# Kernel tuning notes

Measured on AMD Instinct MI355X. Metric: run time of the kernel, lower is better.

Reference implementation:

```python
import jax, jax.numpy as jnp
import numpy as np

NUM_EMBEDDINGS = 2048
EMBEDDING_DIM = 512
INPUT_DIM = 256  # input_chan**2 = 16**2
COMMITMENT_COST = 0.25
BN_EPS = 1e-5


def setup_inputs() -> dict:
    key = jax.random.key(0)
    ks = jax.random.split(key, 8)
    B, N = 64, 1024
    inputs = jax.random.normal(ks[0], (B, N, INPUT_DIM), dtype=jnp.float32)
    # embedding init: uniform(-1/K, 1/K) as in the torch module
    emb_scale = 1.0 / NUM_EMBEDDINGS
    embedding = jax.random.uniform(ks[1], (NUM_EMBEDDINGS, EMBEDDING_DIM), dtype=jnp.float32,
                                   minval=-emb_scale, maxval=emb_scale)
    # Linear layers use torch convention W[out, in]
    W1 = jax.random.normal(ks[2], (EMBEDDING_DIM, INPUT_DIM), dtype=jnp.float32) / np.sqrt(INPUT_DIM)
    b1 = jnp.zeros((EMBEDDING_DIM,), dtype=jnp.float32)
    W2 = jax.random.normal(ks[3], (INPUT_DIM, EMBEDDING_DIM), dtype=jnp.float32) / np.sqrt(EMBEDDING_DIM)
    b2 = jnp.zeros((INPUT_DIM,), dtype=jnp.float32)
    # BatchNorm affine params initialized to 1/0 as in the module
    bn1_gamma = jnp.ones((INPUT_DIM,), dtype=jnp.float32)
    bn1_beta = jnp.zeros((INPUT_DIM,), dtype=jnp.float32)
    bn2_gamma = jnp.ones((EMBEDDING_DIM,), dtype=jnp.float32)
    bn2_beta = jnp.zeros((EMBEDDING_DIM,), dtype=jnp.float32)
    return {"inputs": inputs, "bn1_gamma": bn1_gamma, "bn1_beta": bn1_beta,
            "W1": W1, "b1": b1, "embedding": embedding,
            "bn2_gamma": bn2_gamma, "bn2_beta": bn2_beta, "W2": W2, "b2": b2}


def reference(inputs, bn1_gamma, bn1_beta, W1, b1, embedding, bn2_gamma, bn2_beta, W2, b2):
    sg = jax.lax.stop_gradient
    input_shape = inputs.shape
    flat = inputs.reshape(-1, INPUT_DIM)  # [T, D_in]
    # BatchNorm1d in eval mode (running_mean=0, running_var=1); Dropout is identity in eval.
    bn1_scale = 1.0 / jnp.sqrt(1.0 + BN_EPS)
    x = flat * (bn1_gamma * bn1_scale) + bn1_beta
    x = x @ W1.T + b1  # [T, E]
    # pairwise squared distances to codebook, argmin
    distances = (jnp.sum(x * x, axis=1, keepdims=True)
                 + jnp.sum(embedding * embedding, axis=1)
                 - 2.0 * x @ embedding.T)  # [T, K]
    encoding_indices = jnp.argmin(distances, axis=1)  # [T]
    # gather == one-hot @ embedding (same math, same gradient scatter-add)
    quantized = jnp.take(embedding, encoding_indices, axis=0)  # [T, E]
    bn2_scale = 1.0 / jnp.sqrt(1.0 + BN_EPS)
    quantized = quantized * (bn2_gamma * bn2_scale) + bn2_beta
    quantized = (quantized @ W2.T + b2).reshape(input_shape)
    e_latent_loss = jnp.mean((sg(quantized) - inputs) ** 2)
    q_latent_loss = jnp.mean((quantized - sg(inputs)) ** 2)
    loss = q_latent_loss + COMMITMENT_COST * e_latent_loss
    quantized_st = inputs + sg(quantized - inputs)  # straight-through
    T = flat.shape[0]
    usage = jnp.zeros((NUM_EMBEDDINGS,), dtype=jnp.float32).at[encoding_indices].add(1.0) / T
    return (loss, quantized_st, usage)
```

## Files before the change

### kernel.cpp

```cpp
#include <hip/hip_runtime.h>
#include <math.h>
#include <stdint.h>

#define TOK 65536
#define DIN 256
#define EDIM 512
#define KCB 2048
#define NTB 128

#define OFF_MP   0u
#define OFF_CP   524288u
#define OFF_Q    526336u
#define OFF_W2T  1050624u
#define OFF_U    1181696u
#define OFF_CQ   1182208u
#define OFF_BH   1182464u
#define TOT_F    1444608u

typedef short short8 __attribute__((ext_vector_type(8)));
typedef float f32x4 __attribute__((ext_vector_type(4)));

__device__ __forceinline__ unsigned short bf16rne(float x) {
    uint32_t u = __float_as_uint(x);
    u += 0x7fffu + ((u >> 16) & 1u);
    return (unsigned short)(u >> 16);
}

__global__ void prep1_kernel(const float* __restrict__ W1, const float* __restrict__ W2,
                             const float* __restrict__ bn1_beta, const float* __restrict__ bn2_gamma,
                             const float* __restrict__ bn2_beta, const float* __restrict__ b2,
                             float* __restrict__ W2T, float* __restrict__ u, float* __restrict__ cQ,
                             float* __restrict__ out) {
    __shared__ float red[256];
    const int b = blockIdx.x, t = threadIdx.x;
    const int gid = b * 256 + t;
    if (gid == 0) out[0] = 0.0f;
    if (gid < KCB) out[1 + TOK * DIN + gid] = 0.0f;
    const float s = 1.0f / sqrtf(1.0f + 1e-5f);
    if (b < EDIM) {
        int e = b;
        W2T[e * DIN + t] = bn2_gamma[e] * s * W2[t * EDIM + e];
        float v = bn1_beta[t] * W1[e * DIN + t];
        red[t] = v; __syncthreads();
        for (int off = 128; off; off >>= 1) { if (t < off) red[t] += red[t + off]; __syncthreads(); }
        if (t == 0) u[e] = red[0];
    } else {
        int o = b - EDIM;
        float v = bn2_beta[t] * W2[o * EDIM + t] + bn2_beta[t + 256] * W2[o * EDIM + t + 256];
        red[t] = v; __syncthreads();
        for (int off = 128; off; off >>= 1) { if (t < off) red[t] += red[t + off]; __syncthreads(); }
        if (t == 0) cQ[o] = b2[o] + red[0];
    }
}

__global__ __launch_bounds__(512) void prep2_kernel(const float* __restrict__ E, const float* __restrict__ W1,
                                                    const float* __restrict__ W2T, const float* __restrict__ bn1_gamma,
                                                    const float* __restrict__ cQ, const float* __restrict__ b1,
                                                    const float* __restrict__ u,
                                                    float* __restrict__ Q, float* __restrict__ cp,
                                                    unsigned short* __restrict__ Bh) {
    __shared__ __align__(16) unsigned short hs[8][264];
    const int t = threadIdx.x;
    const int col = t & 255;
    const int half = __builtin_amdgcn_readfirstlane(t >> 8);
    const int k0 = blockIdx.x * 8;
    const float* __restrict__ Ek = E + ((size_t)k0 + (size_t)half * 4) * EDIM;

    float m[4] = {0, 0, 0, 0};
    float q[4] = {0, 0, 0, 0};
    for (int e0 = 0; e0 < EDIM; e0 += 8) {
        float w1v[8], w2v[8];
#pragma unroll
        for (int j = 0; j < 8; j++) {
            w1v[j] = W1[(e0 + j) * DIN + col];
            w2v[j] = W2T[(e0 + j) * DIN + col];
        }
#pragma unroll
        for (int r = 0; r < 4; r++) {
#pragma unroll
            for (int j = 0; j < 8; j++) {
                float ev = Ek[(size_t)r * EDIM + e0 + j];
                m[r] += ev * w1v[j];
                q[r] += ev * w2v[j];
            }
        }
    }
    const float s = 1.0f / sqrtf(1.0f + 1e-5f);
    const float gs = bn1_gamma[col] * s;
    const float cq = cQ[col];
#pragma unroll
    for (int r = 0; r < 4; r++) {
        Q[(size_t)(k0 + half * 4 + r) * DIN + col] = q[r] + cq;
        hs[half * 4 + r][col] = bf16rne(gs * m[r]);
    }

    {
        const int wv = t >> 6, l = t & 63;
        const float* __restrict__ Er = E + (size_t)(k0 + wv) * EDIM;
        float sa = 0.0f, sb = 0.0f;
#pragma unroll
        for (int i = 0; i < 8; i++) {
            int e = l + i * 64;
            float ev = Er[e];
            float be = b1[e] + u[e];
            sa += ev * be; sb += ev * ev;
        }
        float v = sa - 0.5f * sb;
#pragma unroll
        for (int off = 32; off; off >>= 1) v += __shfl_down(v, off, 64);
        if (l == 0) cp[k0 + wv] = v;
    }

    __syncthreads();

    if (t < 256) {
        const int rr = t & 7, qr = (t >> 3) & 3, kc = t >> 5;
        const int nt = k0 >> 4;
        const int l2 = (k0 & 8) + rr + (qr << 4);
        short8 vh = *(const short8*)&hs[rr][kc * 32 + qr * 8];
        *(short8*)&Bh[((size_t)kc * NTB + nt) * 512 + (size_t)l2 * 8] = vh;
    }
}

__global__ __launch_bounds__(256, 2) void score_fused_kernel(const float* __restrict__ flat,
                                                             const unsigned short* __restrict__ Bh,
                                                             const float* __restrict__ cp,
                                                             const float* __restrict__ Q,
                                                             float* __restrict__ out) {
    __shared__ float mv[2][128];
    __shared__ int   mi[2][128];
    const int t = threadIdx.x, lane = t & 63, w = t >> 6;
    const int wr = w >> 1, wc = w & 1;
    const int m0 = blockIdx.x * 128;
    const int fr = lane & 15, qr = lane >> 4;

    short8 af[8][4];
#pragma unroll
    for (int kc = 0; kc < 8; kc++)
#pragma unroll
        for (int mt = 0; mt < 4; mt++) {
            int row = m0 + wr * 64 + mt * 16 + fr;
            const float* p = flat + (size_t)row * DIN + kc * 32 + qr * 8;
            float4 a = *(const float4*)p;
            float4 b = *(const float4*)(p + 4);
            float f[8] = {a.x, a.y, a.z, a.w, b.x, b.y, b.z, b.w};
            unsigned short* hp = (unsigned short*)&af[kc][mt];
#pragma unroll
            for (int j = 0; j < 8; j++) hp[j] = bf16rne(f[j]);
        }

    const unsigned short* __restrict__ Bhaving = Bh + ((size_t)(wc * 64)) * 512 + (size_t)lane * 8;

    float bestv[4][4];
    int besti[4][4];
#pragma unroll
    for (int mt = 0; mt < 4; mt++)
#pragma unroll
        for (int r = 0; r < 4; r++) { bestv[mt][r] = -3.4e38f; besti[mt][r] = 0; }

    const f32x4 ZERO4 = {0.f, 0.f, 0.f, 0.f};

    short8 bf[8];
#pragma unroll
    for (int kc = 0; kc < 8; kc++)
        bf[kc] = *(const short8*)(Bhaving + ((size_t)kc * NTB) * 512);

#pragma unroll 1
    for (int nt = 0; nt < 64; nt++) {
        f32x4 acc[4];
        acc[0] = __builtin_amdgcn_mfma_f32_16x16x32_bf16(af[0][0], bf[0], ZERO4, 0, 0, 0);
        acc[1] = __builtin_amdgcn_mfma_f32_16x16x32_bf16(af[0][1], bf[0], ZERO4, 0, 0, 0);
        acc[2] = __builtin_amdgcn_mfma_f32_16x16x32_bf16(af[0][2], bf[0], ZERO4, 0, 0, 0);
        acc[3] = __builtin_amdgcn_mfma_f32_16x16x32_bf16(af[0][3], bf[0], ZERO4, 0, 0, 0);
#pragma unroll
        for (int kc = 1; kc < 4; kc++) {
#pragma unroll
            for (int mt = 0; mt < 4; mt++)
                acc[mt] = __builtin_amdgcn_mfma_f32_16x16x32_bf16(af[kc][mt], bf[kc], acc[mt], 0, 0, 0);
        }
        if (nt < 63) {
#pragma unroll
            for (int kc = 0; kc < 4; kc++)
                bf[kc] = *(const short8*)(Bhaving + ((size_t)kc * NTB + nt + 1) * 512);
        }
#pragma unroll
        for (int kc = 4; kc < 8; kc++) {
#pragma unroll
            for (int mt = 0; mt < 4; mt++)
                acc[mt] = __builtin_amdgcn_mfma_f32_16x16x32_bf16(af[kc][mt], bf[kc], acc[mt], 0, 0, 0);
        }
        if (nt < 63) {
#pragma unroll
            for (int kc = 4; kc < 8; kc++)
                bf[kc] = *(const short8*)(Bhaving + ((size_t)kc * NTB + nt + 1) * 512);
        }
        const int base = wc * 1024 + nt * 16 + fr;
        const float cpv = cp[base];
#pragma unroll
        for (int mt = 0; mt < 4; mt++)
#pragma unroll
            for (int r = 0; r < 4; r++) {
                float v = acc[mt][r] + cpv;
                if (v > bestv[mt][r]) { bestv[mt][r] = v; besti[mt][r] = base; }
            }
    }

#pragma unroll
    for (int mt = 0; mt < 4; mt++)
#pragma unroll
        for (int r = 0; r < 4; r++) {
            float bv = bestv[mt][r];
            int bc = besti[mt][r];
#pragma unroll
            for (int xm = 1; xm < 16; xm <<= 1) {
                float ov = __shfl_xor(bv, xm, 64);
                int oc = __shfl_xor(bc, xm, 64);
                if (ov > bv || (ov == bv && oc < bc)) { bv = ov; bc = oc; }
            }
            if (fr == 0) {
                int rl = wr * 64 + mt * 16 + qr * 4 + r;
                mv[wc][rl] = bv;
                mi[wc][rl] = bc;
            }
        }
    __syncthreads();

    float lsum = 0.0f;
    for (int rr = 0; rr < 32; rr++) {
        int rl = w * 32 + rr;
        int row = m0 + rl;
        float v0 = mv[0][rl], v1 = mv[1][rl];
        int c0 = mi[0][rl], c1 = mi[1][rl];
        int k = (v1 > v0 || (v1 == v0 && c1 < c0)) ? c1 : c0;
        const float* qr_ = Q + (size_t)k * DIN;
        const float* xr = flat + (size_t)row * DIN;
        float* ob = out + 1 + (size_t)row * DIN;
#pragma unroll
        for (int cc = 0; cc < 4; cc++) {
            int j = lane + 64 * cc;
            float q = qr_[j];
            float d = q - xr[j];
            lsum += d * d;
            ob[j] = q;
        }
        if (lane == 0) atomicAdd(out + 1 + TOK * DIN + k, 1.0f / (float)TOK);
    }
#pragma unroll
    for (int off = 32; off; off >>= 1) lsum += __shfl_down(lsum, off, 64);
    if (lane == 0) atomicAdd(out, lsum * (1.25f / (float)((size_t)TOK * DIN)));
}

extern "C" void kernel_launch(void* const* d_in, const int* in_sizes, int n_in,
                              void* d_out, int out_size, void* d_ws, size_t ws_size,
                              hipStream_t stream) {
    const float* inputs = (const float*)d_in[0];
    const float* bn1_gamma = (const float*)d_in[1];
    const float* bn1_beta  = (const float*)d_in[2];
    const float* W1 = (const float*)d_in[3];
    const float* b1 = (const float*)d_in[4];
    const float* E  = (const float*)d_in[5];
    const float* bn2_gamma = (const float*)d_in[6];
    const float* bn2_beta  = (const float*)d_in[7];
    const float* W2 = (const float*)d_in[8];
    const float* b2 = (const float*)d_in[9];

    float* ws = (float*)d_ws;
    float* cp  = ws + OFF_CP;
    float* Q   = ws + OFF_Q;
    float* W2T = ws + OFF_W2T;
    float* u   = ws + OFF_U;
    float* cQ  = ws + OFF_CQ;
    unsigned short* Bh = (unsigned short*)(ws + OFF_BH);
    float* out = (float*)d_out;

    hipLaunchKernelGGL(prep1_kernel, dim3(768), dim3(256), 0, stream,
                       W1, W2, bn1_beta, bn2_gamma, bn2_beta, b2, W2T, u, cQ, out);
    hipLaunchKernelGGL(prep2_kernel, dim3(256), dim3(512), 0, stream,
                       E, W1, W2T, bn1_gamma, cQ, b1, u, Q, cp, Bh);
    hipLaunchKernelGGL(score_fused_kernel, dim3(512), dim3(256), 0, stream,
                       inputs, Bh, cp, Q, out);
}
```

Before: 272.7 us.

## Shrink score tile to 16 rows per wave across full codebook, raise occupancy

Each wave now computes scores for 16 token rows against all 2048 codes instead of 64 rows against half the codebook. This removes the cross-wave LDS argmin merge and its barrier, cuts the register footprint, and allows 4 blocks per CU with twice the grid. In exchange each B fragment load feeds only one MFMA instead of four, so codebook traffic from L2 rises substantially. A single dependent accumulator chain also reduces MFMA-level parallelism per wave.

```diff
diff --git a/kernel.cpp b/kernel.cpp
--- a/kernel.cpp
+++ b/kernel.cpp
@@ -122,128 +122,105 @@
     }
 }
 
-__global__ __launch_bounds__(256, 2) void score_fused_kernel(const float* __restrict__ flat,
+__global__ __launch_bounds__(256, 4) void score_fused_kernel(const float* __restrict__ flat,
                                                              const unsigned short* __restrict__ Bh,
                                                              const float* __restrict__ cp,
                                                              const float* __restrict__ Q,
                                                              float* __restrict__ out) {
-    __shared__ float mv[2][128];
-    __shared__ int   mi[2][128];
     const int t = threadIdx.x, lane = t & 63, w = t >> 6;
-    const int wr = w >> 1, wc = w & 1;
-    const int m0 = blockIdx.x * 128;
+    const int m0 = blockIdx.x * 64;
     const int fr = lane & 15, qr = lane >> 4;
 
-    short8 af[8][4];
+    short8 af[8];
+#pragma unroll
+    for (int kc = 0; kc < 8; kc++) {
+        int row = m0 + w * 16 + fr;
+        const float* p = flat + (size_t)row * DIN + kc * 32 + qr * 8;
+        float4 a = *(const float4*)p;
+        float4 b = *(const float4*)(p + 4);
+        float f[8] = {a.x, a.y, a.z, a.w, b.x, b.y, b.z, b.w};
+        unsigned short* hp = (unsigned short*)&af[kc];
+#pragma unroll
+        for (int j = 0; j < 8; j++) hp[j] = bf16rne(f[j]);
+    }
+
+    const unsigned short* __restrict__ Bbase = Bh + (size_t)lane * 8;
+
+    float bestv[4];
+    int besti[4];
+#pragma unroll
+    for (int r = 0; r < 4; r++) { bestv[r] = -3.4e38f; besti[r] = 0; }
+
+    const f32x4 ZERO4 = {0.f, 0.f, 0.f, 0.f};
+
+    short8 bf[8];
 #pragma unroll
     for (int kc = 0; kc < 8; kc++)
-#pragma unroll
-        for (int mt = 0; mt < 4; mt++) {
-            int row = m0 + wr * 64 + mt * 16 + fr;
-            const float* p = flat + (size_t)row * DIN + kc * 32 + qr * 8;
-            float4 a = *(const float4*)p;
-            float4 b = *(const float4*)(p + 4);
-            float f[8] = {a.x, a.y, a.z, a.w, b.x, b.y, b.z, b.w};
-            unsigned short* hp = (unsigned short*)&af[kc][mt];
-#pragma unroll
-            for (int j = 0; j < 8; j++) hp[j] = bf16rne(f[j]);
-        }
-
-    const unsigned short* __restrict__ Bhaving = Bh + ((size_t)(wc * 64)) * 512 + (size_t)lane * 8;
-
-    float bestv[4][4];
-    int besti[4][4];
-#pragma unroll
-    for (int mt = 0; mt < 4; mt++)
-#pragma unroll
-        for (int r = 0; r < 4; r++) { bestv[mt][r] = -3.4e38f; besti[mt][r] = 0; }
-
-    const f32x4 ZERO4 = {0.f, 0.f, 0.f, 0.f};
-
-    short8 bf[8];
-#pragma unroll
-    for (int kc = 0; kc < 8; kc++)
-        bf[kc] = *(const short8*)(Bhaving + ((size_t)kc * NTB) * 512);
+        bf[kc] = *(const short8*)(Bbase + ((size_t)kc * NTB) * 512);
 
 #pragma unroll 1
-    for (int nt = 0; nt < 64; nt++) {
-        f32x4 acc[4];
-        acc[0] = __builtin_amdgcn_mfma_f32_16x16x32_bf16(af[0][0], bf[0], ZERO4, 0, 0, 0);
-        acc[1] = __builtin_amdgcn_mfma_f32_16x16x32_bf16(af[0][1], bf[0], ZERO4, 0, 0, 0);
-        acc[2] = __builtin_amdgcn_mfma_f32_16x16x32_bf16(af[0][2], bf[0], ZERO4, 0, 0, 0);
-        acc[3] = __builtin_amdgcn_mfma_f32_16x16x32_bf16(af[0][3], bf[0], ZERO4, 0, 0, 0);
-#pragma unroll
-        for (int kc = 1; kc < 4; kc++) {
-#pragma unroll
-            for (int mt = 0; mt < 4; mt++)
-                acc[mt] = __builtin_amdgcn_mfma_f32_16x16x32_bf16(af[kc][mt], bf[kc], acc[mt], 0, 0, 0);
-        }
-        if (nt < 63) {
+    for (int nt = 0; nt < 128; nt++) {
+        f32x4 acc;
+        acc = __builtin_amdgcn_mfma_f32_16x16x32_bf16(af[0], bf[0], ZERO4, 0, 0, 0);
+#pragma unroll
+        for (int kc = 1; kc < 4; kc++)
+            acc = __builtin_amdgcn_mfma_f32_16x16x32_bf16(af[kc], bf[kc], acc, 0, 0, 0);
+        if (nt < 127) {
 #pragma unroll
             for (int kc = 0; kc < 4; kc++)
-                bf[kc] = *(const short8*)(Bhaving + ((size_t)kc * NTB + nt + 1) * 512);
-        }
-#pragma unroll
-        for (int kc = 4; kc < 8; kc++) {
-#pragma unroll
-            for (int mt = 0; mt < 4; mt++)
-                acc[mt] = __builtin_amdgcn_mfma_f32_16x16x32_bf16(af[kc][mt], bf[kc], acc[mt], 0, 0, 0);
-        }
-        if (nt < 63) {
+                bf[kc] = *(const short8*)(Bbase + ((size_t)kc * NTB + nt + 1) * 512);
+        }
+#pragma unroll
+        for (int kc = 4; kc < 8; kc++)
+            acc = __builtin_amdgcn_mfma_f32_16x16x32_bf16(af[kc], bf[kc], acc, 0, 0, 0);
+        if (nt < 127) {
 #pragma unroll
             for (int kc = 4; kc < 8; kc++)
-                bf[kc] = *(const short8*)(Bhaving + ((size_t)kc * NTB + nt + 1) * 512);
-        }
-        const int base = wc * 1024 + nt * 16 + fr;
+                bf[kc] = *(const short8*)(Bbase + ((size_t)kc * NTB + nt + 1) * 512);
+        }
+        const int base = nt * 16 + fr;
         const float cpv = cp[base];
 #pragma unroll
-        for (int mt = 0; mt < 4; mt++)
-#pragma unroll
-            for (int r = 0; r < 4; r++) {
-                float v = acc[mt][r] + cpv;
-                if (v > bestv[mt][r]) { bestv[mt][r] = v; besti[mt][r] = base; }
+        for (int r = 0; r < 4; r++) {
+            float v = acc[r] + cpv;
+            if (v > bestv[r]) { bestv[r] = v; besti[r] = base; }
+        }
+    }
+
+#pragma unroll
+    for (int r = 0; r < 4; r++) {
+        float bv = bestv[r];
+        int bc = besti[r];
+#pragma unroll
+        for (int xm = 1; xm < 16; xm <<= 1) {
+            float ov = __shfl_xor(bv, xm, 64);
+            int oc = __shfl_xor(bc, xm, 64);
+            if (ov > bv || (ov == bv && oc < bc)) { bv = ov; bc = oc; }
+        }
+        besti[r] = bc;
+    }
+
+    float lsum = 0.0f;
+#pragma unroll
+    for (int rq = 0; rq < 4; rq++) {
+#pragma unroll
+        for (int r = 0; r < 4; r++) {
+            int rr = rq * 4 + r;
+            int row = m0 + w * 16 + rr;
+            int k = __shfl(besti[r], rq * 16, 64);
+            const float* qr_ = Q + (size_t)k * DIN;
+            const float* xr = flat + (size_t)row * DIN;
+            float* ob = out + 1 + (size_t)row * DIN;
+#pragma unroll
+            for (int cc = 0; cc < 4; cc++) {
+                int j = lane + 64 * cc;
+                float q = qr_[j];
+                float d = q - xr[j];
+                lsum += d * d;
+                ob[j] = q;
             }
-    }
-
-#pragma unroll
-    for (int mt = 0; mt < 4; mt++)
-#pragma unroll
-        for (int r = 0; r < 4; r++) {
-            float bv = bestv[mt][r];
-            int bc = besti[mt][r];
-#pragma unroll
-            for (int xm = 1; xm < 16; xm <<= 1) {
-                float ov = __shfl_xor(bv, xm, 64);
-                int oc = __shfl_xor(bc, xm, 64);
-                if (ov > bv || (ov == bv && oc < bc)) { bv = ov; bc = oc; }
-            }
-            if (fr == 0) {
-                int rl = wr * 64 + mt * 16 + qr * 4 + r;
-                mv[wc][rl] = bv;
-                mi[wc][rl] = bc;
-            }
-        }
-    __syncthreads();
-
-    float lsum = 0.0f;
-    for (int rr = 0; rr < 32; rr++) {
-        int rl = w * 32 + rr;
-        int row = m0 + rl;
-        float v0 = mv[0][rl], v1 = mv[1][rl];
-        int c0 = mi[0][rl], c1 = mi[1][rl];
-        int k = (v1 > v0 || (v1 == v0 && c1 < c0)) ? c1 : c0;
-        const float* qr_ = Q + (size_t)k * DIN;
-        const float* xr = flat + (size_t)row * DIN;
-        float* ob = out + 1 + (size_t)row * DIN;
-#pragma unroll
-        for (int cc = 0; cc < 4; cc++) {
-            int j = lane + 64 * cc;
-            float q = qr_[j];
-            float d = q - xr[j];
-            lsum += d * d;
-            ob[j] = q;
-        }
-        if (lane == 0) atomicAdd(out + 1 + TOK * DIN + k, 1.0f / (float)TOK);
+            if (lane == 0) atomicAdd(out + 1 + TOK * DIN + k, 1.0f / (float)TOK);
+        }
     }
 #pragma unroll
     for (int off = 32; off; off >>= 1) lsum += __shfl_down(lsum, off, 64);
@@ -277,6 +254,6 @@
                        W1, W2, bn1_beta, bn2_gamma, bn2_beta, b2, W2T, u, cQ, out);
     hipLaunchKernelGGL(prep2_kernel, dim3(256), dim3(512), 0, stream,
                        E, W1, W2T, bn1_gamma, cQ, b1, u, Q, cp, Bh);
-    hipLaunchKernelGGL(score_fused_kernel, dim3(512), dim3(256), 0, stream,
+    hipLaunchKernelGGL(score_fused_kernel, dim3(1024), dim3(256), 0, stream,
                        inputs, Bh, cp, Q, out);
 }
```

After: 354.7 us. +30.1%, slower.

## Split score and gather into separate kernels and double-buffer codebook tile loads

Applied to the files above, without the earlier changes.

The scoring loop now keeps two register buffers of codebook fragments, so the loads for tile nt+2 are issued while tile nt+1 is being computed, which is meant to hide global-load latency behind the MFMAs. The score kernel now writes only the selected code index per row to workspace. A new gather kernel reads those indices and writes the quantized rows, the loss and the usage counts. This lowers the score kernel's register and tail pressure, at the cost of one extra launch, a round trip of the indices through memory, and re-reading the inputs in a separate pass.

```diff
diff --git a/kernel.cpp b/kernel.cpp
--- a/kernel.cpp
+++ b/kernel.cpp
@@ -8,7 +8,7 @@
 #define KCB 2048
 #define NTB 128
 
-#define OFF_MP   0u
+#define OFF_KSEL 0u
 #define OFF_CP   524288u
 #define OFF_Q    526336u
 #define OFF_W2T  1050624u
@@ -122,11 +122,10 @@
     }
 }
 
-__global__ __launch_bounds__(256, 2) void score_fused_kernel(const float* __restrict__ flat,
-                                                             const unsigned short* __restrict__ Bh,
-                                                             const float* __restrict__ cp,
-                                                             const float* __restrict__ Q,
-                                                             float* __restrict__ out) {
+__global__ __launch_bounds__(256, 2) void score_kernel(const float* __restrict__ flat,
+                                                       const unsigned short* __restrict__ Bh,
+                                                       const float* __restrict__ cp,
+                                                       int* __restrict__ ksel_g) {
     __shared__ float mv[2][128];
     __shared__ int   mi[2][128];
     const int t = threadIdx.x, lane = t & 63, w = t >> 6;
@@ -149,7 +148,7 @@
             for (int j = 0; j < 8; j++) hp[j] = bf16rne(f[j]);
         }
 
-    const unsigned short* __restrict__ Bhaving = Bh + ((size_t)(wc * 64)) * 512 + (size_t)lane * 8;
+    const unsigned short* __restrict__ Bbase = Bh + ((size_t)(wc * 64)) * 512 + (size_t)lane * 8;
 
     float bestv[4][4];
     int besti[4][4];
@@ -160,50 +159,49 @@
 
     const f32x4 ZERO4 = {0.f, 0.f, 0.f, 0.f};
 
-    short8 bf[8];
-#pragma unroll
-    for (int kc = 0; kc < 8; kc++)
-        bf[kc] = *(const short8*)(Bhaving + ((size_t)kc * NTB) * 512);
+#define LOADT(BUF, NTV)                                                              \
+    do { _Pragma("unroll")                                                           \
+        for (int kc_ = 0; kc_ < 8; kc_++)                                            \
+            BUF[kc_] = *(const short8*)(Bbase + ((size_t)kc_ * NTB + (NTV)) * 512);  \
+    } while (0)
+
+#define DO_TILE(BUF, NTV)                                                            \
+    do {                                                                             \
+        f32x4 acc[4];                                                                \
+        _Pragma("unroll")                                                            \
+        for (int mt_ = 0; mt_ < 4; mt_++)                                            \
+            acc[mt_] = __builtin_amdgcn_mfma_f32_16x16x32_bf16(af[0][mt_], BUF[0], ZERO4, 0, 0, 0); \
+        _Pragma("unroll")                                                            \
+        for (int kc_ = 1; kc_ < 8; kc_++) {                                          \
+            _Pragma("unroll")                                                        \
+            for (int mt_ = 0; mt_ < 4; mt_++)                                        \
+                acc[mt_] = __builtin_amdgcn_mfma_f32_16x16x32_bf16(af[kc_][mt_], BUF[kc_], acc[mt_], 0, 0, 0); \
+        }                                                                            \
+        const int base_ = wc * 1024 + (NTV) * 16 + fr;                               \
+        const float cpv_ = cp[base_];                                                \
+        _Pragma("unroll")                                                            \
+        for (int mt_ = 0; mt_ < 4; mt_++) {                                          \
+            _Pragma("unroll")                                                        \
+            for (int r_ = 0; r_ < 4; r_++) {                                         \
+                float v_ = acc[mt_][r_] + cpv_;                                      \
+                if (v_ > bestv[mt_][r_]) { bestv[mt_][r_] = v_; besti[mt_][r_] = base_; } \
+            }                                                                        \
+        }                                                                            \
+    } while (0)
+
+    short8 bfA[8], bfB[8];
+    LOADT(bfA, 0);
+    LOADT(bfB, 1);
 
 #pragma unroll 1
-    for (int nt = 0; nt < 64; nt++) {
-        f32x4 acc[4];
-        acc[0] = __builtin_amdgcn_mfma_f32_16x16x32_bf16(af[0][0], bf[0], ZERO4, 0, 0, 0);
-        acc[1] = __builtin_amdgcn_mfma_f32_16x16x32_bf16(af[0][1], bf[0], ZERO4, 0, 0, 0);
-        acc[2] = __builtin_amdgcn_mfma_f32_16x16x32_bf16(af[0][2], bf[0], ZERO4, 0, 0, 0);
-        acc[3] = __builtin_amdgcn_mfma_f32_16x16x32_bf16(af[0][3], bf[0], ZERO4, 0, 0, 0);
-#pragma unroll
-        for (int kc = 1; kc < 4; kc++) {
-#pragma unroll
-            for (int mt = 0; mt < 4; mt++)
-                acc[mt] = __builtin_amdgcn_mfma_f32_16x16x32_bf16(af[kc][mt], bf[kc], acc[mt], 0, 0, 0);
-        }
-        if (nt < 63) {
-#pragma unroll
-            for (int kc = 0; kc < 4; kc++)
-                bf[kc] = *(const short8*)(Bhaving + ((size_t)kc * NTB + nt + 1) * 512);
-        }
-#pragma unroll
-        for (int kc = 4; kc < 8; kc++) {
-#pragma unroll
-            for (int mt = 0; mt < 4; mt++)
-                acc[mt] = __builtin_amdgcn_mfma_f32_16x16x32_bf16(af[kc][mt], bf[kc], acc[mt], 0, 0, 0);
-        }
-        if (nt < 63) {
-#pragma unroll
-            for (int kc = 4; kc < 8; kc++)
-                bf[kc] = *(const short8*)(Bhaving + ((size_t)kc * NTB + nt + 1) * 512);
-        }
-        const int base = wc * 1024 + nt * 16 + fr;
-        const float cpv = cp[base];
-#pragma unroll
-        for (int mt = 0; mt < 4; mt++)
-#pragma unroll
-            for (int r = 0; r < 4; r++) {
-                float v = acc[mt][r] + cpv;
-                if (v > bestv[mt][r]) { bestv[mt][r] = v; besti[mt][r] = base; }
-            }
-    }
+    for (int nt = 0; nt < 64; nt += 2) {
+        DO_TILE(bfA, nt);
+        if (nt + 2 < 64) LOADT(bfA, nt + 2);
+        DO_TILE(bfB, nt + 1);
+        if (nt + 3 < 64) LOADT(bfB, nt + 3);
+    }
+#undef LOADT
+#undef DO_TILE
 
 #pragma unroll
     for (int mt = 0; mt < 4; mt++)
@@ -225,13 +223,24 @@
         }
     __syncthreads();
 
+    if (t < 128) {
+        float v0 = mv[0][t], v1 = mv[1][t];
+        int c0 = mi[0][t], c1 = mi[1][t];
+        ksel_g[m0 + t] = (v1 > v0 || (v1 == v0 && c1 < c0)) ? c1 : c0;
+    }
+}
+
+__global__ __launch_bounds__(256) void gather_kernel(const float* __restrict__ flat,
+                                                     const float* __restrict__ Q,
+                                                     const int* __restrict__ ksel_g,
+                                                     float* __restrict__ out) {
+    const int t = threadIdx.x, lane = t & 63, w = t >> 6;
+    const int m0 = blockIdx.x * 128;
     float lsum = 0.0f;
     for (int rr = 0; rr < 32; rr++) {
         int rl = w * 32 + rr;
         int row = m0 + rl;
-        float v0 = mv[0][rl], v1 = mv[1][rl];
-        int c0 = mi[0][rl], c1 = mi[1][rl];
-        int k = (v1 > v0 || (v1 == v0 && c1 < c0)) ? c1 : c0;
+        int k = ksel_g[row];
         const float* qr_ = Q + (size_t)k * DIN;
         const float* xr = flat + (size_t)row * DIN;
         float* ob = out + 1 + (size_t)row * DIN;
@@ -265,6 +274,7 @@
     const float* b2 = (const float*)d_in[9];
 
     float* ws = (float*)d_ws;
+    int*   ksel = (int*)(ws + OFF_KSEL);
     float* cp  = ws + OFF_CP;
     float* Q   = ws + OFF_Q;
     float* W2T = ws + OFF_W2T;
@@ -277,6 +287,8 @@
                        W1, W2, bn1_beta, bn2_gamma, bn2_beta, b2, W2T, u, cQ, out);
     hipLaunchKernelGGL(prep2_kernel, dim3(256), dim3(512), 0, stream,
                        E, W1, W2T, bn1_gamma, cQ, b1, u, Q, cp, Bh);
-    hipLaunchKernelGGL(score_fused_kernel, dim3(512), dim3(256), 0, stream,
-                       inputs, Bh, cp, Q, out);
-}
+    hipLaunchKernelGGL(score_kernel, dim3(512), dim3(256), 0, stream,
+                       inputs, Bh, cp, ksel);
+    hipLaunchKernelGGL(gather_kernel, dim3(512), dim3(256), 0, stream,
+                       inputs, Q, ksel, out);
+}
```

New measurement: 339.5 us. 24.5% more time.
